# Optimization experiments

Measured on AMD Instinct MI355X. Metric: run time of the kernel, lower is better.

## Reference

```python
import jax, jax.numpy as jnp
import numpy as np

M = 3          # num_modes
B = 64         # batch
D = 512        # feat_dim
HIST = 5       # history_len (deque pre-filled with HIST zero matrices)
SMOOTH = 0.8   # smooth_factor


def setup_inputs() -> dict:
    ks = jax.random.split(jax.random.key(0), 6)
    return {
        "x": jax.random.normal(ks[0], (M, B, D), jnp.float32),
        "proj_W": jax.random.normal(ks[1], (M, D, D), jnp.float32) * 0.02,
        "proj_b": jnp.zeros((M, D), jnp.float32),
        "ln_g": jnp.ones((M, D), jnp.float32),
        "ln_b": jnp.zeros((M, D), jnp.float32),
        "imp_W1": jax.random.normal(ks[2], (M, D // 4, D), jnp.float32) * 0.02,
        "imp_b1": jnp.zeros((M, D // 4), jnp.float32),
        "imp_W2": jax.random.normal(ks[3], (M, D, D // 4), jnp.float32) * 0.02,
        "imp_b2": jnp.zeros((M, D), jnp.float32),
        "gamma": jax.random.normal(ks[4], (M, M), jnp.float32) * 0.1,
        "modal_bias": jax.random.normal(ks[5], (M, M), jnp.float32) * 0.01,
        "constraint": jnp.ones((M,), jnp.float32) * 0.2,
    }


def _layernorm(v, g, b, eps=1e-5):
    mu = v.mean(-1, keepdims=True)
    var = ((v - mu) ** 2).mean(-1, keepdims=True)
    return (v - mu) / jnp.sqrt(var + eps) * g + b


def reference(x, proj_W, proj_b, ln_g, ln_b, imp_W1, imp_b1, imp_W2, imp_b2,
              gamma, modal_bias, constraint):
    scale = D ** 0.5
    # per-mode projector: Linear -> LayerNorm -> ReLU
    proj = [jax.nn.relu(_layernorm(x[i] @ proj_W[i].T + proj_b[i], ln_g[i], ln_b[i]))
            for i in range(M)]
    # channel importance: Linear -> ReLU -> Linear -> Sigmoid
    cw = [jax.nn.sigmoid(
              jax.nn.relu(proj[i] @ imp_W1[i].T + imp_b1[i]) @ imp_W2[i].T + imp_b2[i])
          for i in range(M)]
    wf = [proj[i] * cw[i] for i in range(M)]  # weighted features [B, D]

    interactions, scores = [], []
    for i in range(M):
        # deque holds HIST zero matrices; appends within this forward replace
        # zeros, so the running mean is sum(appended)/HIST.
        hist_sum = jnp.zeros((D, D), x.dtype)
        hist = hist_sum / HIST
        c = constraint[i]
        feats, gs = [], []
        for j in range(M):
            if i == j:
                continue
            cur = jnp.einsum('bd,be->bde', wf[i], wf[j]) / scale  # [B, D, D]
            constrained = hist + jnp.clip(cur - hist, -c, c)
            final = SMOOTH * constrained + (1.0 - SMOOTH) * cur
            # append detached batch-mean to history
            hist_sum = hist_sum + jax.lax.stop_gradient(final.mean(0))
            hist = hist_sum / HIST
            attn = jax.nn.softmax(final, axis=-1) + modal_bias[i, j]
            g = jax.nn.sigmoid(gamma[i, j])
            attended = jnp.einsum('bde,be->bd', attn, wf[j])  # bmm(attn, value)
            feats.append(g * attended + wf[i])
            gs.append(g)
        interactions.append(jnp.stack(feats).mean(0))
        scores.append(jnp.stack(gs).mean())
    fused = jnp.stack(interactions).mean(0)              # [B, D]
    attention_weights = jax.nn.softmax(jnp.stack(scores))  # [M]
    return fused, attention_weights
```

## Files before the change

### kernel.cpp

```cpp
#include <hip/hip_runtime.h>
#include <math.h>

#define M_ 3
#define B_ 64
#define D_ 512
#define H4 128
#define HIST_ 5
#define BD (B_ * D_)
#define INVSCALE 0.04419417382415922f
#define LOG2E 1.4426950408889634f

__device__ __forceinline__ float wave_sum64(float v) {
#pragma unroll
    for (int o = 32; o >= 1; o >>= 1) v += __shfl_xor(v, o, 64);
    return v;
}

__device__ __forceinline__ float sigmoidf(float x) {
    return 1.0f / (1.0f + __expf(-x));
}

__global__ __launch_bounds__(512) void k_projln(
    const float* __restrict__ x, const float* __restrict__ pW,
    const float* __restrict__ pb, const float* __restrict__ lg,
    const float* __restrict__ lb, const float* __restrict__ W1,
    const float* __restrict__ b1, const float* __restrict__ W2,
    const float* __restrict__ b2, const float* __restrict__ gamma,
    float* __restrict__ wf, float* __restrict__ Ssum,
    float* __restrict__ out)
{
    const int m = blockIdx.x >> 6;
    const int b = blockIdx.x & 63;
    const int t = threadIdx.x;
    __shared__ __align__(16) float xs[D_];
    __shared__ __align__(16) float ps[D_];
    __shared__ __align__(16) float hpart[512];
    __shared__ __align__(16) float hs[H4];
    __shared__ float red[8];

    xs[t] = x[(size_t)(m * B_ + b) * D_ + t];
    __syncthreads();

    const float4* wr = (const float4*)(pW + ((size_t)m * D_ + t) * D_);
    const float4* xv = (const float4*)xs;
    float q[4];
#pragma unroll
    for (int qq = 0; qq < 4; ++qq) {
        float acc = 0.f;
#pragma unroll
        for (int k = 0; k < 32; ++k) {
            const float4 w = wr[(qq << 5) + k];
            const float4 a = xv[(qq << 5) + k];
            acc = fmaf(w.x, a.x, acc); acc = fmaf(w.y, a.y, acc);
            acc = fmaf(w.z, a.z, acc); acc = fmaf(w.w, a.w, acc);
        }
        q[qq] = acc;
    }
    const float y = q[0] + q[1] + q[2] + q[3] + pb[m * D_ + t];

    float s = wave_sum64(y);
    if ((t & 63) == 0) red[t >> 6] = s;
    __syncthreads();
    const float mean = (red[0]+red[1]+red[2]+red[3]+red[4]+red[5]+red[6]+red[7]) * (1.f / D_);
    __syncthreads();
    const float v = y - mean;
    float vs = wave_sum64(v * v);
    if ((t & 63) == 0) red[t >> 6] = vs;
    __syncthreads();
    const float inv = rsqrtf((red[0]+red[1]+red[2]+red[3]+red[4]+red[5]+red[6]+red[7]) * (1.f / D_) + 1e-5f);
    const float p = fmaxf(fmaf(v * inv, lg[m * D_ + t], lb[m * D_ + t]), 0.f);
    ps[t] = p;
    __syncthreads();

    {
        const int r = t & 127, seg = t >> 7;
        const float4* w1 = (const float4*)(W1 + ((size_t)m * H4 + r) * D_) + (seg << 5);
        const float4* pv = (const float4*)ps + (seg << 5);
        float a1 = 0.f;
#pragma unroll
        for (int k = 0; k < 32; ++k) {
            const float4 w = w1[k], pp = pv[k];
            a1 = fmaf(w.x, pp.x, a1); a1 = fmaf(w.y, pp.y, a1);
            a1 = fmaf(w.z, pp.z, a1); a1 = fmaf(w.w, pp.w, a1);
        }
        hpart[t] = a1;
    }
    __syncthreads();
    if (t < H4)
        hs[t] = fmaxf(hpart[t] + hpart[t + 128] + hpart[t + 256] + hpart[t + 384]
                      + b1[m * H4 + t], 0.f);
    __syncthreads();

    const float4* w2 = (const float4*)(W2 + ((size_t)m * D_ + t) * H4);
    const float4* hv = (const float4*)hs;
    float a2 = 0.f;
#pragma unroll
    for (int k = 0; k < H4 / 4; ++k) {
        const float4 w = w2[k], hh = hv[k];
        a2 = fmaf(w.x, hh.x, a2); a2 = fmaf(w.y, hh.y, a2);
        a2 = fmaf(w.z, hh.z, a2); a2 = fmaf(w.w, hh.w, a2);
    }
    const float cw = sigmoidf(a2 + b2[m * D_ + t]);
    const float wv = p * cw;
    wf[(size_t)(m * B_ + b) * D_ + t] = wv;

    float tot = wave_sum64(wv);
    if ((t & 63) == 0) red[t >> 6] = tot;
    __syncthreads();
    if (t == 0)
        Ssum[m * B_ + b] = red[0]+red[1]+red[2]+red[3]+red[4]+red[5]+red[6]+red[7];

    if (blockIdx.x == 0 && t == 0) {
        const float g01 = sigmoidf(gamma[1]), g02 = sigmoidf(gamma[2]);
        const float g10 = sigmoidf(gamma[3]), g12 = sigmoidf(gamma[5]);
        const float g20 = sigmoidf(gamma[6]), g21 = sigmoidf(gamma[7]);
        const float s0 = 0.5f * (g01 + g02);
        const float s1 = 0.5f * (g10 + g12);
        const float s2 = 0.5f * (g20 + g21);
        const float mx = fmaxf(s0, fmaxf(s1, s2));
        const float e0 = __expf(s0 - mx), e1 = __expf(s1 - mx), e2 = __expf(s2 - mx);
        const float den = e0 + e1 + e2;
        out[BD + 0] = e0 / den;
        out[BD + 1] = e1 / den;
        out[BD + 2] = e2 / den;
    }
}

__global__ __launch_bounds__(256) void k_hist(
    const float* __restrict__ wf, const float* __restrict__ cons,
    float* __restrict__ HT)
{
    const int t  = threadIdx.x;
    const int i  = blockIdx.x >> 7;
    const int e0 = (blockIdx.x & 127) << 2;
    const int j  = (i == 0) ? 1 : 0;
    const float c = cons[i];
    const float* wfi = wf + (size_t)i * BD;
    const float* wfj = wf + (size_t)j * BD;

    float h0[4] = {0.f, 0.f, 0.f, 0.f};
    float h1[4] = {0.f, 0.f, 0.f, 0.f};
#pragma unroll 2
    for (int b = 0; b < B_; ++b) {
        const float a0 = wfi[b * D_ + t]       * INVSCALE;
        const float a1 = wfi[b * D_ + t + 256] * INVSCALE;
        const float4 u4 = *(const float4*)(wfj + b * D_ + e0);
        const float uu[4] = {u4.x, u4.y, u4.z, u4.w};
#pragma unroll
        for (int k = 0; k < 4; ++k) {
            float tt = a0 * uu[k]; float mm = fminf(tt, c);
            h0[k] = fmaf(0.8f, mm, fmaf(0.2f, tt, h0[k]));
            tt = a1 * uu[k]; mm = fminf(tt, c);
            h1[k] = fmaf(0.8f, mm, fmaf(0.2f, tt, h1[k]));
        }
    }
    const float hsc = LOG2E / (float)(B_ * HIST_);
    float* r0 = HT + ((size_t)(i << 9) + e0) * D_;
#pragma unroll
    for (int k = 0; k < 4; ++k) {
        r0[(size_t)k * D_ + t]       = h0[k] * hsc;
        r0[(size_t)k * D_ + t + 256] = h1[k] * hsc;
    }
}

__global__ __launch_bounds__(256) void k_pass(
    const float* __restrict__ wf, const float* __restrict__ cons,
    const float* __restrict__ gamma, const float* __restrict__ mbias,
    const float* __restrict__ HT, const float* __restrict__ Ssum,
    float* __restrict__ out)
{
    const int bg   = blockIdx.x >> 4;
    const int dc   = blockIdx.x & 15;
    const int b0   = bg << 1;
    const int t    = threadIdx.x;
    const int ln   = t & 31;
    const int d    = (dc << 5) + ln;
    const int esec = t >> 5;

    __shared__ __align__(16) float4 part[2][256];
    float oacc = 0.f;

#pragma unroll
    for (int i = 0; i < 3; ++i) {
        const int jA = (i == 0) ? 1 : 0;
        const int jB = (i == 2) ? 1 : 2;
        const float c08 = cons[i] * (0.8f * LOG2E);
        const float cl  = cons[i] * LOG2E;

        float a08[2], a02[2], aB[2];
        const float* uA[2];
        const float* uB[2];
#pragma unroll
        for (int bb = 0; bb < 2; ++bb) {
            const float a = wf[(size_t)i * BD + (b0 + bb) * D_ + d];
            a08[bb] = a * (0.8f * INVSCALE * LOG2E);
            a02[bb] = a * (0.2f * INVSCALE * LOG2E);
            aB[bb]  = a * (INVSCALE * LOG2E);
            uA[bb] = wf + (size_t)jA * BD + (b0 + bb) * D_ + (esec << 6);
            uB[bb] = wf + (size_t)jB * BD + (b0 + bb) * D_ + (esec << 6);
        }
        const float* hp = HT + ((size_t)(i << 9) + (esec << 6)) * D_ + d;

        float sA[2] = {0.f, 0.f}, dA[2] = {0.f, 0.f};
        float sB[2] = {0.f, 0.f}, dB[2] = {0.f, 0.f};
#pragma unroll 2
        for (int e = 0; e < 64; e += 4) {
            float hh[4];
#pragma unroll
            for (int k = 0; k < 4; ++k) hh[k] = hp[(size_t)(e + k) * D_];
#pragma unroll
            for (int bb = 0; bb < 2; ++bb) {
                const float4 uA4 = *(const float4*)(uA[bb] + e);
                const float4 uB4 = *(const float4*)(uB[bb] + e);
                const float ua[4] = {uA4.x, uA4.y, uA4.z, uA4.w};
                const float ub[4] = {uB4.x, uB4.y, uB4.z, uB4.w};
#pragma unroll
                for (int k = 0; k < 4; ++k) {
                    const float v1 = a08[bb] * ua[k];
                    const float v2 = fminf(v1, c08);
                    const float fA = fmaf(a02[bb], ua[k], v2);
                    const float pA = __builtin_amdgcn_exp2f(fA);
                    sA[bb] += pA;
                    dA[bb] = fmaf(pA, ua[k], dA[bb]);
                    const float tt = aB[bb] * ub[k];
                    const float df = tt - hh[k];
                    const float mm = fminf(fmaxf(df, -cl), cl);
                    const float fB = fmaf(0.8f, hh[k] + mm, 0.2f * tt);
                    const float pB = __builtin_amdgcn_exp2f(fB);
                    sB[bb] += pB;
                    dB[bb] = fmaf(pB, ub[k], dB[bb]);
                }
            }
        }

        part[0][t] = make_float4(sA[0], dA[0], sB[0], dB[0]);
        part[1][t] = make_float4(sA[1], dA[1], sB[1], dB[1]);
        __syncthreads();
        if (t < 64) {
            const int bb = t >> 5;
            const int l  = t & 31;
            float SsA = 0.f, SdA = 0.f, SsB = 0.f, SdB = 0.f;
#pragma unroll
            for (int k = 0; k < 8; ++k) {
                const float4 pp = part[bb][l + (k << 5)];
                SsA += pp.x; SdA += pp.y; SsB += pp.z; SdB += pp.w;
            }
            const float gA = sigmoidf(gamma[i * 3 + jA]);
            const float gB = sigmoidf(gamma[i * 3 + jB]);
            oacc += gA * (SdA / SsA + mbias[i * 3 + jA] * Ssum[jA * B_ + b0 + bb]);
            oacc += gB * (SdB / SsB + mbias[i * 3 + jB] * Ssum[jB * B_ + b0 + bb]);
        }
        __syncthreads();
    }

    if (t < 64) {
        const int bb = t >> 5;
        const int l  = t & 31;
        const int od = (dc << 5) + l;
        const float w0 = wf[(size_t)0 * BD + (b0 + bb) * D_ + od];
        const float w1 = wf[(size_t)1 * BD + (b0 + bb) * D_ + od];
        const float w2 = wf[(size_t)2 * BD + (b0 + bb) * D_ + od];
        out[(b0 + bb) * D_ + od] = oacc * (1.f / 6.f) + (w0 + w1 + w2) * (1.f / 3.f);
    }
}

extern "C" void kernel_launch(void* const* d_in, const int* in_sizes, int n_in,
                              void* d_out, int out_size, void* d_ws, size_t ws_size,
                              hipStream_t stream) {
    const float* x    = (const float*)d_in[0];
    const float* pW   = (const float*)d_in[1];
    const float* pb   = (const float*)d_in[2];
    const float* lg   = (const float*)d_in[3];
    const float* lb   = (const float*)d_in[4];
    const float* W1   = (const float*)d_in[5];
    const float* b1   = (const float*)d_in[6];
    const float* W2   = (const float*)d_in[7];
    const float* b2   = (const float*)d_in[8];
    const float* gamma= (const float*)d_in[9];
    const float* mb   = (const float*)d_in[10];
    const float* cons = (const float*)d_in[11];
    float* out = (float*)d_out;

    float* ws   = (float*)d_ws;
    float* wf   = ws;
    float* Ssum = ws + 98304;
    float* HT   = ws + 98496;

    k_projln<<<dim3(M_ * B_), dim3(512), 0, stream>>>(x, pW, pb, lg, lb, W1, b1, W2, b2, gamma, wf, Ssum, out);
    k_hist  <<<dim3(384),     dim3(256), 0, stream>>>(wf, cons, HT);
    k_pass  <<<dim3(512),     dim3(256), 0, stream>>>(wf, cons, gamma, mb, HT, Ssum, out);
}
```

Before: 180.3 us.

## Split projection GEMM into tiled kernel and widen batch tile in pass kernel

```diff
diff --git a/kernel.cpp b/kernel.cpp
--- a/kernel.cpp
+++ b/kernel.cpp
@@ -20,9 +20,59 @@
     return 1.0f / (1.0f + __expf(-x));
 }
 
-__global__ __launch_bounds__(512) void k_projln(
+__global__ __launch_bounds__(256) void k_proj(
     const float* __restrict__ x, const float* __restrict__ pW,
-    const float* __restrict__ pb, const float* __restrict__ lg,
+    const float* __restrict__ pb, float* __restrict__ y)
+{
+    const int m   = blockIdx.x >> 7;
+    const int dch = blockIdx.x & 127;
+    const int d0  = dch << 2;
+    const int t   = threadIdx.x;
+    const int dl  = t >> 6;
+    const int bl  = t & 63;
+
+    __shared__ __align__(16) float xs[64][136];
+    __shared__ __align__(16) float ws4[4][128];
+
+    const float* xbase = x + (size_t)m * BD;
+    float part[4];
+
+#pragma unroll
+    for (int q = 0; q < 4; ++q) {
+#pragma unroll
+        for (int j = 0; j < 8; ++j) {
+            const int f  = t + (j << 8);
+            const int b  = f >> 5;
+            const int c4 = f & 31;
+            const float4 v = *(const float4*)(xbase + (size_t)b * D_ + (q << 7) + (c4 << 2));
+            *(float4*)(&xs[b][c4 << 2]) = v;
+        }
+        if (t < 128) {
+            const int r  = t >> 5;
+            const int c4 = t & 31;
+            *(float4*)(&ws4[r][c4 << 2]) =
+                *(const float4*)(pW + ((size_t)m * D_ + d0 + r) * D_ + (q << 7) + (c4 << 2));
+        }
+        __syncthreads();
+
+        float acc = 0.f;
+#pragma unroll
+        for (int c4 = 0; c4 < 32; ++c4) {
+            const float4 w = *(const float4*)(&ws4[dl][c4 << 2]);
+            const float4 a = *(const float4*)(&xs[bl][c4 << 2]);
+            acc = fmaf(w.x, a.x, acc); acc = fmaf(w.y, a.y, acc);
+            acc = fmaf(w.z, a.z, acc); acc = fmaf(w.w, a.w, acc);
+        }
+        part[q] = acc;
+        __syncthreads();
+    }
+
+    const float yv = ((part[0] + part[1]) + part[2]) + part[3] + pb[m * D_ + d0 + dl];
+    y[(size_t)(m * B_ + bl) * D_ + d0 + dl] = yv;
+}
+
+__global__ __launch_bounds__(512) void k_lnmlp(
+    const float* __restrict__ y, const float* __restrict__ lg,
     const float* __restrict__ lb, const float* __restrict__ W1,
     const float* __restrict__ b1, const float* __restrict__ W2,
     const float* __restrict__ b2, const float* __restrict__ gamma,
@@ -32,38 +82,19 @@
     const int m = blockIdx.x >> 6;
     const int b = blockIdx.x & 63;
     const int t = threadIdx.x;
-    __shared__ __align__(16) float xs[D_];
     __shared__ __align__(16) float ps[D_];
+    __shared__ __align__(16) float hs[H4];
     __shared__ __align__(16) float hpart[512];
-    __shared__ __align__(16) float hs[H4];
     __shared__ float red[8];
 
-    xs[t] = x[(size_t)(m * B_ + b) * D_ + t];
-    __syncthreads();
-
-    const float4* wr = (const float4*)(pW + ((size_t)m * D_ + t) * D_);
-    const float4* xv = (const float4*)xs;
-    float q[4];
-#pragma unroll
-    for (int qq = 0; qq < 4; ++qq) {
-        float acc = 0.f;
-#pragma unroll
-        for (int k = 0; k < 32; ++k) {
-            const float4 w = wr[(qq << 5) + k];
-            const float4 a = xv[(qq << 5) + k];
-            acc = fmaf(w.x, a.x, acc); acc = fmaf(w.y, a.y, acc);
-            acc = fmaf(w.z, a.z, acc); acc = fmaf(w.w, a.w, acc);
-        }
-        q[qq] = acc;
-    }
-    const float y = q[0] + q[1] + q[2] + q[3] + pb[m * D_ + t];
-
-    float s = wave_sum64(y);
+    const float yv = y[(size_t)(m * B_ + b) * D_ + t];
+
+    float s = wave_sum64(yv);
     if ((t & 63) == 0) red[t >> 6] = s;
     __syncthreads();
     const float mean = (red[0]+red[1]+red[2]+red[3]+red[4]+red[5]+red[6]+red[7]) * (1.f / D_);
     __syncthreads();
-    const float v = y - mean;
+    const float v = yv - mean;
     float vs = wave_sum64(v * v);
     if ((t & 63) == 0) red[t >> 6] = vs;
     __syncthreads();
@@ -171,13 +202,13 @@
 {
     const int bg   = blockIdx.x >> 4;
     const int dc   = blockIdx.x & 15;
-    const int b0   = bg << 1;
+    const int b0   = bg << 2;
     const int t    = threadIdx.x;
     const int ln   = t & 31;
     const int d    = (dc << 5) + ln;
     const int esec = t >> 5;
 
-    __shared__ __align__(16) float4 part[2][256];
+    __shared__ __align__(16) float4 part[4][256];
     float oacc = 0.f;
 
 #pragma unroll
@@ -187,11 +218,11 @@
         const float c08 = cons[i] * (0.8f * LOG2E);
         const float cl  = cons[i] * LOG2E;
 
-        float a08[2], a02[2], aB[2];
-        const float* uA[2];
-        const float* uB[2];
-#pragma unroll
-        for (int bb = 0; bb < 2; ++bb) {
+        float a08[4], a02[4], aB[4];
+        const float* uA[4];
+        const float* uB[4];
+#pragma unroll
+        for (int bb = 0; bb < 4; ++bb) {
             const float a = wf[(size_t)i * BD + (b0 + bb) * D_ + d];
             a08[bb] = a * (0.8f * INVSCALE * LOG2E);
             a02[bb] = a * (0.2f * INVSCALE * LOG2E);
@@ -201,15 +232,15 @@
         }
         const float* hp = HT + ((size_t)(i << 9) + (esec << 6)) * D_ + d;
 
-        float sA[2] = {0.f, 0.f}, dA[2] = {0.f, 0.f};
-        float sB[2] = {0.f, 0.f}, dB[2] = {0.f, 0.f};
+        float sA[4] = {0.f, 0.f, 0.f, 0.f}, dA[4] = {0.f, 0.f, 0.f, 0.f};
+        float sB[4] = {0.f, 0.f, 0.f, 0.f}, dB[4] = {0.f, 0.f, 0.f, 0.f};
 #pragma unroll 2
         for (int e = 0; e < 64; e += 4) {
             float hh[4];
 #pragma unroll
             for (int k = 0; k < 4; ++k) hh[k] = hp[(size_t)(e + k) * D_];
 #pragma unroll
-            for (int bb = 0; bb < 2; ++bb) {
+            for (int bb = 0; bb < 4; ++bb) {
                 const float4 uA4 = *(const float4*)(uA[bb] + e);
                 const float4 uB4 = *(const float4*)(uB[bb] + e);
                 const float ua[4] = {uA4.x, uA4.y, uA4.z, uA4.w};
@@ -233,10 +264,11 @@
             }
         }
 
-        part[0][t] = make_float4(sA[0], dA[0], sB[0], dB[0]);
-        part[1][t] = make_float4(sA[1], dA[1], sB[1], dB[1]);
+#pragma unroll
+        for (int bb = 0; bb < 4; ++bb)
+            part[bb][t] = make_float4(sA[bb], dA[bb], sB[bb], dB[bb]);
         __syncthreads();
-        if (t < 64) {
+        if (t < 128) {
             const int bb = t >> 5;
             const int l  = t & 31;
             float SsA = 0.f, SdA = 0.f, SsB = 0.f, SdB = 0.f;
@@ -253,7 +285,7 @@
         __syncthreads();
     }
 
-    if (t < 64) {
+    if (t < 128) {
         const int bb = t >> 5;
         const int l  = t & 31;
         const int od = (dc << 5) + l;
@@ -285,8 +317,10 @@
     float* wf   = ws;
     float* Ssum = ws + 98304;
     float* HT   = ws + 98496;
-
-    k_projln<<<dim3(M_ * B_), dim3(512), 0, stream>>>(x, pW, pb, lg, lb, W1, b1, W2, b2, gamma, wf, Ssum, out);
-    k_hist  <<<dim3(384),     dim3(256), 0, stream>>>(wf, cons, HT);
-    k_pass  <<<dim3(512),     dim3(256), 0, stream>>>(wf, cons, gamma, mb, HT, Ssum, out);
-}
+    float* y    = ws + 884928;
+
+    k_proj <<<dim3(384),     dim3(256), 0, stream>>>(x, pW, pb, y);
+    k_lnmlp<<<dim3(M_ * B_), dim3(512), 0, stream>>>(y, lg, lb, W1, b1, W2, b2, gamma, wf, Ssum, out);
+    k_hist <<<dim3(384),     dim3(256), 0, stream>>>(wf, cons, HT);
+    k_pass <<<dim3(256),     dim3(256), 0, stream>>>(wf, cons, gamma, mb, HT, Ssum, out);
+}
```

After: 239.7 us. +33.0%, slower.

## Coalesce projector GEMV weight reads and process four batches per pass block

Applied to the files above, without the earlier changes.

```diff
diff --git a/kernel.cpp b/kernel.cpp
--- a/kernel.cpp
+++ b/kernel.cpp
@@ -13,6 +13,12 @@
 __device__ __forceinline__ float wave_sum64(float v) {
 #pragma unroll
     for (int o = 32; o >= 1; o >>= 1) v += __shfl_xor(v, o, 64);
+    return v;
+}
+
+__device__ __forceinline__ float half_sum32(float v) {
+#pragma unroll
+    for (int o = 16; o >= 1; o >>= 1) v += __shfl_xor(v, o, 64);
     return v;
 }
 
@@ -32,32 +38,41 @@
     const int m = blockIdx.x >> 6;
     const int b = blockIdx.x & 63;
     const int t = threadIdx.x;
+    const int w = t >> 6;
+    const int l = t & 63;
+
     __shared__ __align__(16) float xs[D_];
+    __shared__ __align__(16) float ys[D_];
     __shared__ __align__(16) float ps[D_];
-    __shared__ __align__(16) float hpart[512];
     __shared__ __align__(16) float hs[H4];
     __shared__ float red[8];
 
     xs[t] = x[(size_t)(m * B_ + b) * D_ + t];
     __syncthreads();
 
-    const float4* wr = (const float4*)(pW + ((size_t)m * D_ + t) * D_);
-    const float4* xv = (const float4*)xs;
-    float q[4];
-#pragma unroll
-    for (int qq = 0; qq < 4; ++qq) {
-        float acc = 0.f;
-#pragma unroll
-        for (int k = 0; k < 32; ++k) {
-            const float4 w = wr[(qq << 5) + k];
-            const float4 a = xv[(qq << 5) + k];
-            acc = fmaf(w.x, a.x, acc); acc = fmaf(w.y, a.y, acc);
-            acc = fmaf(w.z, a.z, acc); acc = fmaf(w.w, a.w, acc);
-        }
-        q[qq] = acc;
-    }
-    const float y = q[0] + q[1] + q[2] + q[3] + pb[m * D_ + t];
-
+    {
+        const float4* xv = (const float4*)xs;
+        const float4 xa = xv[l];
+        const float4 xb = xv[64 + l];
+        const float* wbase = pW + (size_t)m * D_ * D_;
+#pragma unroll 2
+        for (int dd = 0; dd < 64; ++dd) {
+            const int d = (w << 6) + dd;
+            const float4* wr = (const float4*)(wbase + (size_t)d * D_);
+            const float4 wa = wr[l];
+            const float4 wb = wr[64 + l];
+            float acc;
+            acc = wa.x * xa.x;            acc = fmaf(wa.y, xa.y, acc);
+            acc = fmaf(wa.z, xa.z, acc);  acc = fmaf(wa.w, xa.w, acc);
+            acc = fmaf(wb.x, xb.x, acc);  acc = fmaf(wb.y, xb.y, acc);
+            acc = fmaf(wb.z, xb.z, acc);  acc = fmaf(wb.w, xb.w, acc);
+            acc = wave_sum64(acc);
+            if (l == 0) ys[d] = acc;
+        }
+    }
+    __syncthreads();
+
+    const float y = ys[t] + pb[m * D_ + t];
     float s = wave_sum64(y);
     if ((t & 63) == 0) red[t >> 6] = s;
     __syncthreads();
@@ -73,34 +88,47 @@
     __syncthreads();
 
     {
-        const int r = t & 127, seg = t >> 7;
-        const float4* w1 = (const float4*)(W1 + ((size_t)m * H4 + r) * D_) + (seg << 5);
-        const float4* pv = (const float4*)ps + (seg << 5);
-        float a1 = 0.f;
-#pragma unroll
-        for (int k = 0; k < 32; ++k) {
-            const float4 w = w1[k], pp = pv[k];
-            a1 = fmaf(w.x, pp.x, a1); a1 = fmaf(w.y, pp.y, a1);
-            a1 = fmaf(w.z, pp.z, a1); a1 = fmaf(w.w, pp.w, a1);
-        }
-        hpart[t] = a1;
-    }
-    __syncthreads();
-    if (t < H4)
-        hs[t] = fmaxf(hpart[t] + hpart[t + 128] + hpart[t + 256] + hpart[t + 384]
-                      + b1[m * H4 + t], 0.f);
-    __syncthreads();
-
-    const float4* w2 = (const float4*)(W2 + ((size_t)m * D_ + t) * H4);
-    const float4* hv = (const float4*)hs;
-    float a2 = 0.f;
-#pragma unroll
-    for (int k = 0; k < H4 / 4; ++k) {
-        const float4 w = w2[k], hh = hv[k];
-        a2 = fmaf(w.x, hh.x, a2); a2 = fmaf(w.y, hh.y, a2);
-        a2 = fmaf(w.z, hh.z, a2); a2 = fmaf(w.w, hh.w, a2);
-    }
-    const float cw = sigmoidf(a2 + b2[m * D_ + t]);
+        const float4* pv = (const float4*)ps;
+        const float4 pa = pv[l];
+        const float4 pbv = pv[64 + l];
+        const float* w1base = W1 + (size_t)m * H4 * D_;
+#pragma unroll 2
+        for (int rr = 0; rr < 16; ++rr) {
+            const int r = (w << 4) + rr;
+            const float4* wr = (const float4*)(w1base + (size_t)r * D_);
+            const float4 wa = wr[l];
+            const float4 wb = wr[64 + l];
+            float acc;
+            acc = wa.x * pa.x;            acc = fmaf(wa.y, pa.y, acc);
+            acc = fmaf(wa.z, pa.z, acc);  acc = fmaf(wa.w, pa.w, acc);
+            acc = fmaf(wb.x, pbv.x, acc); acc = fmaf(wb.y, pbv.y, acc);
+            acc = fmaf(wb.z, pbv.z, acc); acc = fmaf(wb.w, pbv.w, acc);
+            acc = wave_sum64(acc);
+            if (l == 0) hs[r] = fmaxf(acc + b1[m * H4 + r], 0.f);
+        }
+    }
+    __syncthreads();
+
+    {
+        const float4* hv = (const float4*)hs;
+        const float4 hc = hv[l & 31];
+        const int half = l >> 5;
+        const float* w2base = W2 + (size_t)m * D_ * H4;
+#pragma unroll 2
+        for (int s2 = 0; s2 < 32; ++s2) {
+            const int r = (w << 6) + (s2 << 1) + half;
+            const float4* wr = (const float4*)(w2base + (size_t)r * H4);
+            const float4 w4 = wr[l & 31];
+            float acc;
+            acc = w4.x * hc.x;            acc = fmaf(w4.y, hc.y, acc);
+            acc = fmaf(w4.z, hc.z, acc);  acc = fmaf(w4.w, hc.w, acc);
+            acc = half_sum32(acc);
+            if ((l & 31) == 0) ys[r] = acc;
+        }
+    }
+    __syncthreads();
+
+    const float cw = sigmoidf(ys[t] + b2[m * D_ + t]);
     const float wv = p * cw;
     wf[(size_t)(m * B_ + b) * D_ + t] = wv;
 
@@ -171,13 +199,13 @@
 {
     const int bg   = blockIdx.x >> 4;
     const int dc   = blockIdx.x & 15;
-    const int b0   = bg << 1;
+    const int b0   = bg << 2;
     const int t    = threadIdx.x;
     const int ln   = t & 31;
     const int d    = (dc << 5) + ln;
     const int esec = t >> 5;
 
-    __shared__ __align__(16) float4 part[2][256];
+    __shared__ __align__(16) float4 part[4][256];
     float oacc = 0.f;
 
 #pragma unroll
@@ -187,11 +215,11 @@
         const float c08 = cons[i] * (0.8f * LOG2E);
         const float cl  = cons[i] * LOG2E;
 
-        float a08[2], a02[2], aB[2];
-        const float* uA[2];
-        const float* uB[2];
-#pragma unroll
-        for (int bb = 0; bb < 2; ++bb) {
+        float a08[4], a02[4], aB[4];
+        const float* uA[4];
+        const float* uB[4];
+#pragma unroll
+        for (int bb = 0; bb < 4; ++bb) {
             const float a = wf[(size_t)i * BD + (b0 + bb) * D_ + d];
             a08[bb] = a * (0.8f * INVSCALE * LOG2E);
             a02[bb] = a * (0.2f * INVSCALE * LOG2E);
@@ -201,15 +229,15 @@
         }
         const float* hp = HT + ((size_t)(i << 9) + (esec << 6)) * D_ + d;
 
-        float sA[2] = {0.f, 0.f}, dA[2] = {0.f, 0.f};
-        float sB[2] = {0.f, 0.f}, dB[2] = {0.f, 0.f};
+        float sA[4] = {0.f, 0.f, 0.f, 0.f}, dA[4] = {0.f, 0.f, 0.f, 0.f};
+        float sB[4] = {0.f, 0.f, 0.f, 0.f}, dB[4] = {0.f, 0.f, 0.f, 0.f};
 #pragma unroll 2
         for (int e = 0; e < 64; e += 4) {
             float hh[4];
 #pragma unroll
             for (int k = 0; k < 4; ++k) hh[k] = hp[(size_t)(e + k) * D_];
 #pragma unroll
-            for (int bb = 0; bb < 2; ++bb) {
+            for (int bb = 0; bb < 4; ++bb) {
                 const float4 uA4 = *(const float4*)(uA[bb] + e);
                 const float4 uB4 = *(const float4*)(uB[bb] + e);
                 const float ua[4] = {uA4.x, uA4.y, uA4.z, uA4.w};
@@ -233,10 +261,11 @@
             }
         }
 
-        part[0][t] = make_float4(sA[0], dA[0], sB[0], dB[0]);
-        part[1][t] = make_float4(sA[1], dA[1], sB[1], dB[1]);
+#pragma unroll
+        for (int bb = 0; bb < 4; ++bb)
+            part[bb][t] = make_float4(sA[bb], dA[bb], sB[bb], dB[bb]);
         __syncthreads();
-        if (t < 64) {
+        if (t < 128) {
             const int bb = t >> 5;
             const int l  = t & 31;
             float SsA = 0.f, SdA = 0.f, SsB = 0.f, SdB = 0.f;
@@ -253,7 +282,7 @@
         __syncthreads();
     }
 
-    if (t < 64) {
+    if (t < 128) {
         const int bb = t >> 5;
         const int l  = t & 31;
         const int od = (dc << 5) + l;
@@ -288,5 +317,5 @@
 
     k_projln<<<dim3(M_ * B_), dim3(512), 0, stream>>>(x, pW, pb, lg, lb, W1, b1, W2, b2, gamma, wf, Ssum, out);
     k_hist  <<<dim3(384),     dim3(256), 0, stream>>>(wf, cons, HT);
-    k_pass  <<<dim3(512),     dim3(256), 0, stream>>>(wf, cons, gamma, mb, HT, Ssum, out);
-}
+    k_pass  <<<dim3(256),     dim3(256), 0, stream>>>(wf, cons, gamma, mb, HT, Ssum, out);
+}
```

After: 198.1 us. 9.9% more time.
